# Performance work log

Hardware: AMD Instinct MI355X
Metric: run time of the kernel (lower is better)

## Reference

```python
import jax, jax.numpy as jnp
import numpy as np

N_NODE = 100000
HIDDEN = 128
BATCH = 4096
SESS_LEN = 50


def setup_inputs() -> dict:
    key = jax.random.key(0)
    k1, k2, k3, k4, k5 = jax.random.split(key, 5)
    return {
        "item_embedding": jax.random.normal(k1, (N_NODE, HIDDEN), dtype=jnp.float32),
        "items": jax.random.randint(k2, (BATCH, SESS_LEN), 0, N_NODE, dtype=jnp.int64),
        "A": jax.random.uniform(k3, (BATCH, BATCH), dtype=jnp.float32),
        "D": jax.random.uniform(k4, (BATCH, BATCH), dtype=jnp.float32),
        "target_embedding": jax.random.normal(k5, (BATCH, 1, 2 * HIDDEN), dtype=jnp.float32),
    }


def reference(item_embedding, items, A, D, target_embedding):
    # Gather per-session item embeddings: (batch, sess_len, hidden)
    seq_h = item_embedding[items]
    # Sum over session positions -> (batch, hidden)
    relation_emb = jnp.sum(seq_h, axis=1)
    # DA = D @ A, then propagate: (batch, batch) @ (batch, hidden)
    DA = jnp.matmul(D, A)
    relation_emb = jnp.matmul(DA, relation_emb)
    # Row-wise L2 normalization (torch.norm(dim=-1))
    norm = jnp.linalg.norm(relation_emb, axis=-1, keepdims=True)
    return relation_emb / norm
```

## Files before the change

kernel.cpp:

```cpp
#include <hip/hip_runtime.h>
#include <hip/hip_bf16.h>

#define BATCH   4096
#define HIDDEN  128
#define SESS    50
#define KTOT    4096
#define NB      ((size_t)BATCH * HIDDEN)

typedef __bf16 bf16x8 __attribute__((ext_vector_type(8)));
typedef float  f32x4  __attribute__((ext_vector_type(4)));
typedef unsigned char uchar;

__device__ __forceinline__ f32x4 mfma_bf16(bf16x8 a, bf16x8 b, f32x4 c) {
    return __builtin_amdgcn_mfma_f32_16x16x32_bf16(a, b, c, 0, 0, 0);
}

__device__ __forceinline__ long packBH(int k, int h) {
    return ((long)(k >> 3) << 10) + ((h >> 4) << 7) + ((h & 15) << 3) + (k & 7);
}

__global__ __launch_bounds__(64)
void probe_kernel(int* __restrict__ flag, uchar* __restrict__ rtab,
                  uchar* __restrict__ ctab) {
    __shared__ float As[16][32];
    __shared__ float Bs[32][16];
    __shared__ int cnt[256];
    const int lane = threadIdx.x;
    for (int idx = lane; idx < 512; idx += 64) {
        const int m = idx >> 5, k = idx & 31;
        As[m][k] = (float)(((m * 5 + k * 3) % 17) - 8);
        const int kb = idx >> 4, n = idx & 15;
        Bs[kb][n] = (float)(((kb * 7 + n * 11) % 17) - 8);
    }
    for (int i = lane; i < 256; i += 64) cnt[i] = 0;
    __syncthreads();

    const int lo = lane & 15, quad = lane >> 4;
    bf16x8 a, b, a1, b1, a2, b2;
#pragma unroll
    for (int j = 0; j < 8; ++j) {
        a[j]  = (__bf16)As[lo][quad * 8 + j];
        b[j]  = (__bf16)Bs[quad * 8 + j][lo];
        a1[j] = (__bf16)0.f; b1[j] = (__bf16)0.f;
        a2[j] = (__bf16)0.f; b2[j] = (__bf16)0.f;
    }
    if (quad == 0) {
        a1[0] = (__bf16)(float)lo;  b1[0] = (__bf16)1.f;
        a2[0] = (__bf16)1.f;        b2[0] = (__bf16)(float)lo;
    }
    const f32x4 z = {0.f, 0.f, 0.f, 0.f};
    f32x4 d  = mfma_bf16(a,  b,  z);
    f32x4 d1 = mfma_bf16(a1, b1, z);
    f32x4 d2 = mfma_bf16(a2, b2, z);

    bool ok = true;
    int ms[4], ns[4];
#pragma unroll
    for (int r = 0; r < 4; ++r) {
        const int m = (int)d1[r], n = (int)d2[r];
        ok = ok && ((float)m == d1[r]) && ((float)n == d2[r]) &&
             (m >= 0) && (m < 16) && (n >= 0) && (n < 16);
        ms[r] = m & 15; ns[r] = n & 15;
        float ref = 0.f;
        for (int k = 0; k < 32; ++k) ref += As[ms[r]][k] * Bs[k][ns[r]];
        ok = ok && (d[r] == ref);
        atomicAdd(&cnt[ms[r] * 16 + ns[r]], 1);
    }
    __syncthreads();
    bool comp = true;
    for (int i = lane; i < 256; i += 64) comp = comp && (cnt[i] == 1);

    const unsigned long long b_ok   = __ballot(ok);
    const unsigned long long b_comp = __ballot(comp);
#pragma unroll
    for (int r = 0; r < 4; ++r) {
        rtab[lane * 4 + r] = (uchar)ms[r];
        ctab[lane * 4 + r] = (uchar)ns[r];
    }
    if (lane == 0)
        *flag = (b_ok == ~0ULL && b_comp == ~0ULL) ? 1 : 0;
}

__global__ __launch_bounds__(256)
void gather_sum_kernel(const float* __restrict__ emb,
                       const int* __restrict__ items32,
                       float* __restrict__ Ef,
                       __bf16* __restrict__ ETp) {
    __shared__ int sidx[2][SESS];
    __shared__ f32x4 red[2][4][32];
    const int t  = threadIdx.x;
    const int b0 = blockIdx.x * 2;
    const bool is64 = (items32[1] | items32[3] | items32[5] | items32[7] |
                       items32[9] | items32[11] | items32[13] | items32[15]) == 0;
    if (t < 2 * SESS) {
        sidx[t / SESS][t % SESS] =
            is64 ? (int)((const long long*)items32)[(long)b0 * SESS + t]
                 : items32[b0 * SESS + t];
    }
    __syncthreads();
    const int r  = t >> 7;
    const int g  = (t >> 5) & 3;
    const int c4 = (t & 31) * 4;
    f32x4 acc = {0.f, 0.f, 0.f, 0.f};
#pragma unroll
    for (int s = g; s < SESS; s += 4) {
        acc += *(const f32x4*)(emb + (long)sidx[r][s] * HIDDEN + c4);
    }
    red[r][g][t & 31] = acc;
    __syncthreads();
    if (g == 0) {
        const int b = b0 + r;
        const f32x4 v = red[r][0][t & 31] + red[r][1][t & 31] +
                        red[r][2][t & 31] + red[r][3][t & 31];
        *(f32x4*)(Ef + (long)b * HIDDEN + c4) = v;
        const long pb = ((long)(b >> 3) << 10) + (b & 7) + ((c4 >> 4) << 7);
#pragma unroll
        for (int j = 0; j < 4; ++j)
            ETp[pb + ((c4 & 15) + j) * 8] = (__bf16)v[j];
    }
}

template <int PHASE>
__global__ __launch_bounds__(256, 4)
void gemm_mfma_kernel(const float* __restrict__ X,
                      const __bf16* __restrict__ BTp,
                      const int* __restrict__ flag,
                      const uchar* __restrict__ rtab,
                      const uchar* __restrict__ ctab,
                      float* __restrict__ Tp,
                      float* __restrict__ RpX) {
    if (*flag != 1) return;
    __shared__ float red[4][16][128];

    const int tid  = threadIdx.x;
    const int wave = tid >> 6;
    const int lane = tid & 63;
    const int lo   = lane & 15;
    const int quad = lane >> 4;
    const int rowBase = blockIdx.x * 16;
    const int sy      = blockIdx.y;
    const int kBase   = sy * 1024 + wave * 256;

    const unsigned rt4 = ((const unsigned*)rtab)[lane];
    const unsigned ct4 = ((const unsigned*)ctab)[lane];

    f32x4 acc[8];
#pragma unroll
    for (int i = 0; i < 8; ++i) acc[i] = (f32x4){0.f, 0.f, 0.f, 0.f};

    const float*  ap = X + (long)(rowBase + lo) * KTOT + kBase + quad * 8;
    const __bf16* bp = BTp + (((long)(kBase >> 3) + quad) << 10) + lo * 8;

    f32x4 x0 = *(const f32x4*)(ap);
    f32x4 x1 = *(const f32x4*)(ap + 4);
    bf16x8 bb[8];
#pragma unroll
    for (int nt = 0; nt < 8; ++nt)
        bb[nt] = *(const bf16x8*)(bp + nt * 128);

#pragma unroll
    for (int it = 0; it < 7; ++it) {
        const float*  ap2 = ap + (it + 1) * 32;
        const __bf16* bp2 = bp + (long)(it + 1) * 4096;
        const f32x4 nx0 = *(const f32x4*)(ap2);
        const f32x4 nx1 = *(const f32x4*)(ap2 + 4);
        bf16x8 nb[8];
#pragma unroll
        for (int nt = 0; nt < 8; ++nt)
            nb[nt] = *(const bf16x8*)(bp2 + nt * 128);
        bf16x8 a;
        a[0] = (__bf16)x0[0]; a[1] = (__bf16)x0[1];
        a[2] = (__bf16)x0[2]; a[3] = (__bf16)x0[3];
        a[4] = (__bf16)x1[0]; a[5] = (__bf16)x1[1];
        a[6] = (__bf16)x1[2]; a[7] = (__bf16)x1[3];
#pragma unroll
        for (int nt = 0; nt < 8; ++nt)
            acc[nt] = mfma_bf16(a, bb[nt], acc[nt]);
        x0 = nx0; x1 = nx1;
#pragma unroll
        for (int nt = 0; nt < 8; ++nt) bb[nt] = nb[nt];
    }
    {
        bf16x8 a;
        a[0] = (__bf16)x0[0]; a[1] = (__bf16)x0[1];
        a[2] = (__bf16)x0[2]; a[3] = (__bf16)x0[3];
        a[4] = (__bf16)x1[0]; a[5] = (__bf16)x1[1];
        a[6] = (__bf16)x1[2]; a[7] = (__bf16)x1[3];
#pragma unroll
        for (int nt = 0; nt < 8; ++nt)
            acc[nt] = mfma_bf16(a, bb[nt], acc[nt]);
    }

#pragma unroll
    for (int r = 0; r < 4; ++r) {
        const int dr = (rt4 >> (8 * r)) & 255;
        const int dc = (ct4 >> (8 * r)) & 255;
#pragma unroll
        for (int nt = 0; nt < 8; ++nt)
            red[wave][dr][nt * 16 + dc] = acc[nt][r];
    }
    __syncthreads();

    float* outp = (PHASE == 1) ? (Tp + (size_t)sy * NB)
                               : (sy < 3 ? Tp + (size_t)(sy + 1) * NB : RpX);
    const int row = tid >> 4;
    const int cb  = (tid & 15) * 8;
    f32x4 v0, v1;
#pragma unroll
    for (int j = 0; j < 4; ++j) {
        v0[j] = red[0][row][cb + j] + red[1][row][cb + j] +
                red[2][row][cb + j] + red[3][row][cb + j];
        v1[j] = red[0][row][cb + 4 + j] + red[1][row][cb + 4 + j] +
                red[2][row][cb + 4 + j] + red[3][row][cb + 4 + j];
    }
    *(f32x4*)(outp + (long)(rowBase + row) * HIDDEN + cb)     = v0;
    *(f32x4*)(outp + (long)(rowBase + row) * HIDDEN + cb + 4) = v1;
}

template <int PHASE>
__global__ __launch_bounds__(256)
void gemm_fp32_kernel(const float* __restrict__ X,
                      const float* __restrict__ B,
                      const int* __restrict__ flag,
                      float* __restrict__ Tp,
                      float* __restrict__ RpX) {
    if (*flag == 1) return;
    const int tid = threadIdx.x;
    const int cg4 = (tid & 31) * 4;
    const int rg  = tid >> 5;
    const int r0  = blockIdx.x * 32 + rg * 4;
    const int sy  = blockIdx.y;
    const int ks  = sy * 1024;
    float* outp = (PHASE == 1) ? (Tp + (size_t)sy * NB)
                               : (sy < 3 ? Tp + (size_t)(sy + 1) * NB : RpX);

    f32x4 acc[4];
#pragma unroll
    for (int j = 0; j < 4; ++j) acc[j] = (f32x4){0.f, 0.f, 0.f, 0.f};

    const float* Bp = B + (long)ks * HIDDEN + cg4;
    const float* Xp = X + (long)r0 * KTOT + ks;

    for (int k = 0; k < 1024; k += 4) {
        const f32x4 b0 = *(const f32x4*)(Bp + (long)(k + 0) * HIDDEN);
        const f32x4 b1 = *(const f32x4*)(Bp + (long)(k + 1) * HIDDEN);
        const f32x4 b2 = *(const f32x4*)(Bp + (long)(k + 2) * HIDDEN);
        const f32x4 b3 = *(const f32x4*)(Bp + (long)(k + 3) * HIDDEN);
#pragma unroll
        for (int j = 0; j < 4; ++j) {
            const f32x4 x = *(const f32x4*)(Xp + (long)j * KTOT + k);
            acc[j] += x[0] * b0;
            acc[j] += x[1] * b1;
            acc[j] += x[2] * b2;
            acc[j] += x[3] * b3;
        }
    }
#pragma unroll
    for (int j = 0; j < 4; ++j)
        *(f32x4*)(outp + (long)(r0 + j) * HIDDEN + cg4) = acc[j];
}

__global__ __launch_bounds__(256)
void reduce4_kernel(float* __restrict__ Tp, __bf16* __restrict__ TTp) {
    const size_t i = ((size_t)blockIdx.x * 256 + threadIdx.x) * 4;
    f32x4 a = *(const f32x4*)(Tp + i);
    a += *(const f32x4*)(Tp + NB + i);
    a += *(const f32x4*)(Tp + 2 * NB + i);
    a += *(const f32x4*)(Tp + 3 * NB + i);
    *(f32x4*)(Tp + i) = a;
    const int b  = (int)(i >> 7);
    const int h0 = (int)(i & 127);
    const long pb = ((long)(b >> 3) << 10) + (b & 7) + ((h0 >> 4) << 7);
#pragma unroll
    for (int j = 0; j < 4; ++j)
        TTp[pb + ((h0 & 15) + j) * 8] = (__bf16)a[j];
}

__global__ __launch_bounds__(128)
void reduce_norm_kernel(const float* __restrict__ Tp,
                        const float* __restrict__ RpX,
                        float* __restrict__ out) {
    __shared__ float s[128];
    const int row = blockIdx.x;
    const int h   = threadIdx.x;
    const size_t i = (size_t)row * HIDDEN + h;
    const float v = Tp[NB + i] + Tp[2 * NB + i] + Tp[3 * NB + i] + RpX[i];
    s[h] = v * v;
    __syncthreads();
#pragma unroll
    for (int o = 64; o > 0; o >>= 1) {
        if (h < o) s[h] += s[h + o];
        __syncthreads();
    }
    out[i] = v * rsqrtf(s[0]);
}

extern "C" void kernel_launch(void* const* d_in, const int* in_sizes, int n_in,
                              void* d_out, int out_size, void* d_ws, size_t ws_size,
                              hipStream_t stream) {
    const float* emb   = (const float*)d_in[0];
    const int*   items = (const int*)d_in[1];
    const float* A     = (const float*)d_in[2];
    const float* D     = (const float*)d_in[3];
    float* out = (float*)d_out;

    uchar* base = (uchar*)d_ws;
    int*   flag = (int*)base;
    uchar* rtab = base + 64;
    uchar* ctab = base + 320;
    float*  Ef  = (float*)(base + 1024);
    __bf16* ETp = (__bf16*)(Ef + NB);
    __bf16* TTp = ETp + NB;
    float*  Tp  = (float*)(TTp + NB);
    float*  RpX = Tp + 4 * NB;

    probe_kernel<<<1, 64, 0, stream>>>(flag, rtab, ctab);
    gather_sum_kernel<<<BATCH / 2, 256, 0, stream>>>(emb, items, Ef, ETp);

    gemm_mfma_kernel<1><<<dim3(BATCH / 16, 4), 256, 0, stream>>>(A, ETp, flag, rtab, ctab, Tp, RpX);
    gemm_fp32_kernel<1><<<dim3(BATCH / 32, 4), 256, 0, stream>>>(A, Ef, flag, Tp, RpX);
    reduce4_kernel<<<512, 256, 0, stream>>>(Tp, TTp);

    gemm_mfma_kernel<2><<<dim3(BATCH / 16, 4), 256, 0, stream>>>(D, TTp, flag, rtab, ctab, Tp, RpX);
    gemm_fp32_kernel<2><<<dim3(BATCH / 32, 4), 256, 0, stream>>>(D, Tp, flag, Tp, RpX);
    reduce_norm_kernel<<<BATCH, 128, 0, stream>>>(Tp, RpX, out);
}
```

Measured before the change: 238.7 us.

## Restructure MFMA GEMM to single-wave 32-row tiles with 16-way split-K

The MFMA GEMM moves from 256-thread blocks that reduce four wave partials through shared memory to 64-thread single-wave blocks. Each block computes 32 rows, so every B fragment feeds two MFMAs, and K is split 16 ways so each block writes its partial directly to global memory. Separate reduction kernels then sum the 16 partials, with fp32-fallback variants kept alongside. This drops the LDS reduction and barrier and doubles B reuse per load, at the cost of much larger partial-sum traffic (16 slices of BATCH×HIDDEN) and two extra launches.

```diff
diff --git a/kernel.cpp b/kernel.cpp
--- a/kernel.cpp
+++ b/kernel.cpp
@@ -5,6 +5,7 @@
 #define HIDDEN  128
 #define SESS    50
 #define KTOT    4096
+#define NSPL    16
 #define NB      ((size_t)BATCH * HIDDEN)
 
 typedef __bf16 bf16x8 __attribute__((ext_vector_type(8)));
@@ -15,9 +16,6 @@
     return __builtin_amdgcn_mfma_f32_16x16x32_bf16(a, b, c, 0, 0, 0);
 }
 
-__device__ __forceinline__ long packBH(int k, int h) {
-    return ((long)(k >> 3) << 10) + ((h >> 4) << 7) + ((h & 15) << 3) + (k & 7);
-}
 
 __global__ __launch_bounds__(64)
 void probe_kernel(int* __restrict__ flag, uchar* __restrict__ rtab,
@@ -120,110 +118,118 @@
     }
 }
 
-template <int PHASE>
-__global__ __launch_bounds__(256, 4)
+__global__ __launch_bounds__(64, 2)
 void gemm_mfma_kernel(const float* __restrict__ X,
                       const __bf16* __restrict__ BTp,
                       const int* __restrict__ flag,
                       const uchar* __restrict__ rtab,
                       const uchar* __restrict__ ctab,
-                      float* __restrict__ Tp,
-                      float* __restrict__ RpX) {
+                      float* __restrict__ Pp) {
     if (*flag != 1) return;
-    __shared__ float red[4][16][128];
-
-    const int tid  = threadIdx.x;
-    const int wave = tid >> 6;
-    const int lane = tid & 63;
+    const int lane = threadIdx.x;
     const int lo   = lane & 15;
     const int quad = lane >> 4;
-    const int rowBase = blockIdx.x * 16;
-    const int sy      = blockIdx.y;
-    const int kBase   = sy * 1024 + wave * 256;
+    const int r0   = blockIdx.x * 32;
+    const int sy   = blockIdx.y;
+    const int kb   = sy * 256;
 
     const unsigned rt4 = ((const unsigned*)rtab)[lane];
     const unsigned ct4 = ((const unsigned*)ctab)[lane];
 
-    f32x4 acc[8];
-#pragma unroll
-    for (int i = 0; i < 8; ++i) acc[i] = (f32x4){0.f, 0.f, 0.f, 0.f};
-
-    const float*  ap = X + (long)(rowBase + lo) * KTOT + kBase + quad * 8;
-    const __bf16* bp = BTp + (((long)(kBase >> 3) + quad) << 10) + lo * 8;
-
-    f32x4 x0 = *(const f32x4*)(ap);
-    f32x4 x1 = *(const f32x4*)(ap + 4);
-    bf16x8 bb[8];
-#pragma unroll
-    for (int nt = 0; nt < 8; ++nt)
-        bb[nt] = *(const bf16x8*)(bp + nt * 128);
-
-#pragma unroll
-    for (int it = 0; it < 7; ++it) {
-        const float*  ap2 = ap + (it + 1) * 32;
-        const __bf16* bp2 = bp + (long)(it + 1) * 4096;
-        const f32x4 nx0 = *(const f32x4*)(ap2);
-        const f32x4 nx1 = *(const f32x4*)(ap2 + 4);
-        bf16x8 nb[8];
+    f32x4 acc0[8], acc1[8];
+#pragma unroll
+    for (int i = 0; i < 8; ++i) {
+        acc0[i] = (f32x4){0.f, 0.f, 0.f, 0.f};
+        acc1[i] = (f32x4){0.f, 0.f, 0.f, 0.f};
+    }
+
+    const float*  ap0 = X + (long)(r0 + lo) * KTOT + kb + quad * 8;
+    const float*  ap1 = ap0 + 16 * KTOT;
+    const __bf16* bp  = BTp + (((long)(kb >> 3) + quad) << 10) + lo * 8;
+
+#pragma unroll
+    for (int it = 0; it < 8; ++it) {
+        const f32x4 x00 = *(const f32x4*)(ap0 + it * 32);
+        const f32x4 x01 = *(const f32x4*)(ap0 + it * 32 + 4);
+        const f32x4 x10 = *(const f32x4*)(ap1 + it * 32);
+        const f32x4 x11 = *(const f32x4*)(ap1 + it * 32 + 4);
+        bf16x8 b[8];
 #pragma unroll
         for (int nt = 0; nt < 8; ++nt)
-            nb[nt] = *(const bf16x8*)(bp2 + nt * 128);
-        bf16x8 a;
-        a[0] = (__bf16)x0[0]; a[1] = (__bf16)x0[1];
-        a[2] = (__bf16)x0[2]; a[3] = (__bf16)x0[3];
-        a[4] = (__bf16)x1[0]; a[5] = (__bf16)x1[1];
-        a[6] = (__bf16)x1[2]; a[7] = (__bf16)x1[3];
-#pragma unroll
-        for (int nt = 0; nt < 8; ++nt)
-            acc[nt] = mfma_bf16(a, bb[nt], acc[nt]);
-        x0 = nx0; x1 = nx1;
-#pragma unroll
-        for (int nt = 0; nt < 8; ++nt) bb[nt] = nb[nt];
-    }
-    {
-        bf16x8 a;
-        a[0] = (__bf16)x0[0]; a[1] = (__bf16)x0[1];
-        a[2] = (__bf16)x0[2]; a[3] = (__bf16)x0[3];
-        a[4] = (__bf16)x1[0]; a[5] = (__bf16)x1[1];
-        a[6] = (__bf16)x1[2]; a[7] = (__bf16)x1[3];
-#pragma unroll
-        for (int nt = 0; nt < 8; ++nt)
-            acc[nt] = mfma_bf16(a, bb[nt], acc[nt]);
-    }
-
+            b[nt] = *(const bf16x8*)(bp + (long)it * 4096 + nt * 128);
+        bf16x8 a0, a1;
+        a0[0] = (__bf16)x00[0]; a0[1] = (__bf16)x00[1];
+        a0[2] = (__bf16)x00[2]; a0[3] = (__bf16)x00[3];
+        a0[4] = (__bf16)x01[0]; a0[5] = (__bf16)x01[1];
+        a0[6] = (__bf16)x01[2]; a0[7] = (__bf16)x01[3];
+        a1[0] = (__bf16)x10[0]; a1[1] = (__bf16)x10[1];
+        a1[2] = (__bf16)x10[2]; a1[3] = (__bf16)x10[3];
+        a1[4] = (__bf16)x11[0]; a1[5] = (__bf16)x11[1];
+        a1[6] = (__bf16)x11[2]; a1[7] = (__bf16)x11[3];
+#pragma unroll
+        for (int nt = 0; nt < 8; ++nt) {
+            acc0[nt] = mfma_bf16(a0, b[nt], acc0[nt]);
+            acc1[nt] = mfma_bf16(a1, b[nt], acc1[nt]);
+        }
+    }
+
+    float* outp = Pp + (size_t)sy * NB;
 #pragma unroll
     for (int r = 0; r < 4; ++r) {
         const int dr = (rt4 >> (8 * r)) & 255;
         const int dc = (ct4 >> (8 * r)) & 255;
 #pragma unroll
-        for (int nt = 0; nt < 8; ++nt)
-            red[wave][dr][nt * 16 + dc] = acc[nt][r];
-    }
-    __syncthreads();
-
-    float* outp = (PHASE == 1) ? (Tp + (size_t)sy * NB)
-                               : (sy < 3 ? Tp + (size_t)(sy + 1) * NB : RpX);
-    const int row = tid >> 4;
-    const int cb  = (tid & 15) * 8;
-    f32x4 v0, v1;
-#pragma unroll
-    for (int j = 0; j < 4; ++j) {
-        v0[j] = red[0][row][cb + j] + red[1][row][cb + j] +
-                red[2][row][cb + j] + red[3][row][cb + j];
-        v1[j] = red[0][row][cb + 4 + j] + red[1][row][cb + 4 + j] +
-                red[2][row][cb + 4 + j] + red[3][row][cb + 4 + j];
-    }
-    *(f32x4*)(outp + (long)(rowBase + row) * HIDDEN + cb)     = v0;
-    *(f32x4*)(outp + (long)(rowBase + row) * HIDDEN + cb + 4) = v1;
-}
-
-template <int PHASE>
+        for (int nt = 0; nt < 8; ++nt) {
+            outp[(long)(r0 + dr) * HIDDEN + nt * 16 + dc]      = acc0[nt][r];
+            outp[(long)(r0 + 16 + dr) * HIDDEN + nt * 16 + dc] = acc1[nt][r];
+        }
+    }
+}
+
+__global__ __launch_bounds__(256)
+void reduce16_kernel(const float* __restrict__ Pp, const int* __restrict__ flag,
+                     __bf16* __restrict__ TTp) {
+    if (*flag != 1) return;
+    const size_t i = ((size_t)blockIdx.x * 256 + threadIdx.x) * 4;
+    f32x4 a = {0.f, 0.f, 0.f, 0.f};
+#pragma unroll
+    for (int s = 0; s < NSPL; ++s)
+        a += *(const f32x4*)(Pp + (size_t)s * NB + i);
+    const int b  = (int)(i >> 7);
+    const int h0 = (int)(i & 127);
+    const long pb = ((long)(b >> 3) << 10) + (b & 7) + ((h0 >> 4) << 7);
+#pragma unroll
+    for (int j = 0; j < 4; ++j)
+        TTp[pb + ((h0 & 15) + j) * 8] = (__bf16)a[j];
+}
+
+__global__ __launch_bounds__(128)
+void reduce_norm16_kernel(const float* __restrict__ Rp,
+                          const int* __restrict__ flag,
+                          float* __restrict__ out) {
+    if (*flag != 1) return;
+    __shared__ float s[128];
+    const int row = blockIdx.x;
+    const int h   = threadIdx.x;
+    const size_t i = (size_t)row * HIDDEN + h;
+    float v = 0.f;
+#pragma unroll
+    for (int k = 0; k < NSPL; ++k) v += Rp[(size_t)k * NB + i];
+    s[h] = v * v;
+    __syncthreads();
+#pragma unroll
+    for (int o = 64; o > 0; o >>= 1) {
+        if (h < o) s[h] += s[h + o];
+        __syncthreads();
+    }
+    out[i] = v * rsqrtf(s[0]);
+}
+
 __global__ __launch_bounds__(256)
 void gemm_fp32_kernel(const float* __restrict__ X,
                       const float* __restrict__ B,
                       const int* __restrict__ flag,
-                      float* __restrict__ Tp,
-                      float* __restrict__ RpX) {
+                      float* __restrict__ Q) {
     if (*flag == 1) return;
     const int tid = threadIdx.x;
     const int cg4 = (tid & 31) * 4;
@@ -231,8 +237,7 @@
     const int r0  = blockIdx.x * 32 + rg * 4;
     const int sy  = blockIdx.y;
     const int ks  = sy * 1024;
-    float* outp = (PHASE == 1) ? (Tp + (size_t)sy * NB)
-                               : (sy < 3 ? Tp + (size_t)(sy + 1) * NB : RpX);
+    float* outp = Q + (size_t)sy * NB;
 
     f32x4 acc[4];
 #pragma unroll
@@ -261,30 +266,27 @@
 }
 
 __global__ __launch_bounds__(256)
-void reduce4_kernel(float* __restrict__ Tp, __bf16* __restrict__ TTp) {
+void reduce4f_kernel(const float* __restrict__ Q, const int* __restrict__ flag,
+                     float* __restrict__ Tf) {
+    if (*flag == 1) return;
     const size_t i = ((size_t)blockIdx.x * 256 + threadIdx.x) * 4;
-    f32x4 a = *(const f32x4*)(Tp + i);
-    a += *(const f32x4*)(Tp + NB + i);
-    a += *(const f32x4*)(Tp + 2 * NB + i);
-    a += *(const f32x4*)(Tp + 3 * NB + i);
-    *(f32x4*)(Tp + i) = a;
-    const int b  = (int)(i >> 7);
-    const int h0 = (int)(i & 127);
-    const long pb = ((long)(b >> 3) << 10) + (b & 7) + ((h0 >> 4) << 7);
-#pragma unroll
-    for (int j = 0; j < 4; ++j)
-        TTp[pb + ((h0 & 15) + j) * 8] = (__bf16)a[j];
+    f32x4 a = *(const f32x4*)(Q + i);
+    a += *(const f32x4*)(Q + NB + i);
+    a += *(const f32x4*)(Q + 2 * NB + i);
+    a += *(const f32x4*)(Q + 3 * NB + i);
+    *(f32x4*)(Tf + i) = a;
 }
 
 __global__ __launch_bounds__(128)
-void reduce_norm_kernel(const float* __restrict__ Tp,
-                        const float* __restrict__ RpX,
-                        float* __restrict__ out) {
+void reduce_norm4f_kernel(const float* __restrict__ Q,
+                          const int* __restrict__ flag,
+                          float* __restrict__ out) {
+    if (*flag == 1) return;
     __shared__ float s[128];
     const int row = blockIdx.x;
     const int h   = threadIdx.x;
     const size_t i = (size_t)row * HIDDEN + h;
-    const float v = Tp[NB + i] + Tp[2 * NB + i] + Tp[3 * NB + i] + RpX[i];
+    const float v = Q[i] + Q[NB + i] + Q[2 * NB + i] + Q[3 * NB + i];
     s[h] = v * v;
     __syncthreads();
 #pragma unroll
@@ -308,20 +310,25 @@
     int*   flag = (int*)base;
     uchar* rtab = base + 64;
     uchar* ctab = base + 320;
-    float*  Ef  = (float*)(base + 1024);
-    __bf16* ETp = (__bf16*)(Ef + NB);
-    __bf16* TTp = ETp + NB;
-    float*  Tp  = (float*)(TTp + NB);
-    float*  RpX = Tp + 4 * NB;
+    float*  Ef   = (float*)(base + 1024);
+    __bf16* ETp  = (__bf16*)(Ef + NB);
+    __bf16* TTp  = ETp + NB;
+    float*  Tp16 = (float*)(TTp + NB);
+    float*  Rp16 = Tp16 + NSPL * NB;
+    float*  Tf   = Rp16 + NSPL * NB;
+    float*  Tq   = Tf + NB;
+    float*  Rq   = Tq + 4 * NB;
 
     probe_kernel<<<1, 64, 0, stream>>>(flag, rtab, ctab);
     gather_sum_kernel<<<BATCH / 2, 256, 0, stream>>>(emb, items, Ef, ETp);
 
-    gemm_mfma_kernel<1><<<dim3(BATCH / 16, 4), 256, 0, stream>>>(A, ETp, flag, rtab, ctab, Tp, RpX);
-    gemm_fp32_kernel<1><<<dim3(BATCH / 32, 4), 256, 0, stream>>>(A, Ef, flag, Tp, RpX);
-    reduce4_kernel<<<512, 256, 0, stream>>>(Tp, TTp);
-
-    gemm_mfma_kernel<2><<<dim3(BATCH / 16, 4), 256, 0, stream>>>(D, TTp, flag, rtab, ctab, Tp, RpX);
-    gemm_fp32_kernel<2><<<dim3(BATCH / 32, 4), 256, 0, stream>>>(D, Tp, flag, Tp, RpX);
-    reduce_norm_kernel<<<BATCH, 128, 0, stream>>>(Tp, RpX, out);
-}
+    gemm_mfma_kernel<<<dim3(BATCH / 32, NSPL), 64, 0, stream>>>(A, ETp, flag, rtab, ctab, Tp16);
+    gemm_fp32_kernel<<<dim3(BATCH / 32, 4), 256, 0, stream>>>(A, Ef, flag, Tq);
+    reduce16_kernel<<<512, 256, 0, stream>>>(Tp16, flag, TTp);
+    reduce4f_kernel<<<512, 256, 0, stream>>>(Tq, flag, Tf);
+
+    gemm_mfma_kernel<<<dim3(BATCH / 32, NSPL), 64, 0, stream>>>(D, TTp, flag, rtab, ctab, Rp16);
+    gemm_fp32_kernel<<<dim3(BATCH / 32, 4), 256, 0, stream>>>(D, Tf, flag, Rq);
+    reduce_norm16_kernel<<<BATCH, 128, 0, stream>>>(Rp16, flag, out);
+    reduce_norm4f_kernel<<<BATCH, 128, 0, stream>>>(Rq, flag, out);
+}
```

After: 253.9 us. +6.4%, slower.
